# Kernel tuning notes

Measured on AMD Instinct MI355X. Metric: run time of the kernel, lower is better.

## Reference

```python
import jax, jax.numpy as jnp
import numpy as np

EPS = 1e-5

def _conv1x1(x, w):
    # w: [out_ch, in_ch], x: [n, c, h, w] -> [n, out_ch, h, w]
    return jnp.einsum('oc,nchw->nohw', w, x)

def _bn_relu(x, g, b, m, v):
    # inference-mode BatchNorm2d followed by ReLU
    s = g * jax.lax.rsqrt(v + EPS)
    return jax.nn.relu(x * s[None, :, None, None] + (b - m * s)[None, :, None, None])

def setup_inputs() -> dict:
    N, C, H, W, Kc, K = 8, 512, 128, 128, 512, 19
    keys = iter(jax.random.split(jax.random.key(0), 64))
    d = {}
    d['x'] = jax.random.normal(next(keys), (N, C, H, W), jnp.float32)
    d['proxy'] = jax.random.normal(next(keys), (N, C, K, 1), jnp.float32)
    for nm, shp in [('wp1', (Kc, C)), ('wp2', (Kc, Kc)), ('wo1', (Kc, C)),
                    ('wo2', (Kc, Kc)), ('wd', (Kc, C)), ('wu', (C, Kc))]:
        d[nm] = jax.random.normal(next(keys), shp, jnp.float32) * np.float32(1.0 / np.sqrt(shp[1]))
    for tag, ch in [('p1', Kc), ('p2', Kc), ('o1', Kc), ('o2', Kc), ('d', Kc), ('u', C)]:
        d['g' + tag] = 1.0 + 0.1 * jax.random.normal(next(keys), (ch,), jnp.float32)
        d['b' + tag] = 0.1 * jax.random.normal(next(keys), (ch,), jnp.float32)
        d['m' + tag] = 0.1 * jax.random.normal(next(keys), (ch,), jnp.float32)
        d['v' + tag] = jax.random.uniform(next(keys), (ch,), jnp.float32, 0.5, 1.5)
    return d

def reference(x, proxy,
              wp1, gp1, bp1, mp1, vp1, wp2, gp2, bp2, mp2, vp2,
              wo1, go1, bo1, mo1, vo1, wo2, go2, bo2, mo2, vo2,
              wd, gd, bd, md, vd, wu, gu, bu, mu, vu):
    # scale == 1: no pooling / upsampling
    # f_pixel: two 1x1 conv + BN + ReLU on pixel features
    q = _bn_relu(_conv1x1(x, wp1), gp1, bp1, mp1, vp1)
    q = _bn_relu(_conv1x1(q, wp2), gp2, bp2, mp2, vp2)        # [n, kc, h, w]
    n, kc, h, w = q.shape
    q = q.reshape(n, kc, h * w)                               # [n, kc, hw]
    # f_object on proxy (object region representations)
    k = _bn_relu(_conv1x1(proxy, wo1), go1, bo1, mo1, vo1)
    k = _bn_relu(_conv1x1(k, wo2), go2, bo2, mo2, vo2).reshape(n, kc, -1)  # [n, kc, K]
    # f_down (value)
    v = _bn_relu(_conv1x1(proxy, wd), gd, bd, md, vd).reshape(n, kc, -1)   # [n, kc, K]
    # cross-attention: pixels attend over object regions
    sim = jnp.einsum('ncq,nck->nqk', q, k) * (kc ** -0.5)     # [n, hw, K]
    attn = jax.nn.softmax(sim, axis=-1)
    ctx = jnp.einsum('nqk,nck->ncq', attn, v).reshape(n, kc, h, w)
    # f_up: 1x1 conv + BN + ReLU back to in_channels
    return _bn_relu(_conv1x1(ctx, wu), gu, bu, mu, vu)
```

## Files before the change

### kernel.cpp

```cpp
#include <hip/hip_runtime.h>
#include <stdint.h>

#define HW 16384
#define CH 512
#define KR 19

typedef float f32x4 __attribute__((ext_vector_type(4)));
typedef _Float16 half8 __attribute__((ext_vector_type(8)));
typedef unsigned short us8 __attribute__((ext_vector_type(8)));

__device__ __forceinline__ unsigned short f2h(float f) {
    union { _Float16 h; unsigned short u; } v; v.h = (_Float16)f; return v.u;
}
__device__ __forceinline__ float h2f(unsigned short u) {
    union { unsigned short u; _Float16 h; } v; v.u = u; return (float)v.h;
}

__global__ void ObjectAttentionBlock_1176821039805_kernel() {}

__global__ __launch_bounds__(256) void prep_kernel(
    const float* __restrict__ wp1, const float* __restrict__ wp2, const float* __restrict__ wu,
    unsigned short* __restrict__ wp1h, unsigned short* __restrict__ wp2h, unsigned short* __restrict__ wuh,
    const float* gp1, const float* bp1, const float* mp1, const float* vp1,
    const float* gp2, const float* bp2, const float* mp2, const float* vp2,
    const float* gu,  const float* bu,  const float* mu,  const float* vu,
    float* __restrict__ cons)
{
    int i = blockIdx.x * 256 + threadIdx.x;
    if (i < CH * CH) {
        wp1h[i] = f2h(wp1[i]);
        wp2h[i] = f2h(wp2[i]);
        wuh[i]  = f2h(wu[i]);
    }
    if (i < CH) {
        float s1 = gp1[i] * rsqrtf(vp1[i] + 1e-5f);
        cons[i] = s1;          cons[512 + i]  = bp1[i] - mp1[i] * s1;
        float s2 = gp2[i] * rsqrtf(vp2[i] + 1e-5f);
        cons[1024 + i] = s2;   cons[1536 + i] = bp2[i] - mp2[i] * s2;
        float su = gu[i] * rsqrtf(vu[i] + 1e-5f);
        cons[2048 + i] = su;   cons[2560 + i] = bu[i] - mu[i] * su;
    }
}

__global__ __launch_bounds__(256) void transpose_kernel(
    const float* __restrict__ x, unsigned short* __restrict__ xT)
{
    __shared__ unsigned short t[64][66];
    const int n  = blockIdx.z;
    const int c0 = blockIdx.y * 64;
    const int m0 = blockIdx.x * 64;
    const int tx = threadIdx.x & 63;
    const int ty = threadIdx.x >> 6;
    const float* xb = x + ((size_t)n * CH + c0) * HW + m0;
    #pragma unroll
    for (int r = 0; r < 16; ++r) {
        int cl = ty * 16 + r;
        t[cl][tx] = f2h(xb[(size_t)cl * HW + tx]);
    }
    __syncthreads();
    unsigned short* xo = xT + ((size_t)n * HW + m0) * CH + c0;
    #pragma unroll
    for (int r = 0; r < 16; ++r) {
        int ml = ty * 16 + r;
        xo[(size_t)ml * CH + tx] = t[tx][ml];
    }
}

__global__ __launch_bounds__(256) void kv1_kernel(
    const float* __restrict__ proxy, const float* __restrict__ wo1, const float* __restrict__ wd,
    const float* go1, const float* bo1, const float* mo1, const float* vo1,
    const float* gd,  const float* bd,  const float* md,  const float* vd,
    float* __restrict__ t1, float* __restrict__ vout)
{
    const int n  = blockIdx.x;
    const int o0 = blockIdx.y * 64;
    const float* px = proxy + (size_t)n * CH * KR;
    for (int idx = threadIdx.x; idx < 64 * KR; idx += 256) {
        int o = o0 + idx / KR;
        int j = idx % KR;
        float a1 = 0.f, a2 = 0.f;
        for (int c = 0; c < CH; ++c) {
            float p = px[c * KR + j];
            a1 += wo1[o * CH + c] * p;
            a2 += wd [o * CH + c] * p;
        }
        float s1 = go1[o] * rsqrtf(vo1[o] + 1e-5f);
        float s2 = gd[o]  * rsqrtf(vd[o]  + 1e-5f);
        t1  [((size_t)n * CH + o) * KR + j] = fmaxf(a1 * s1 + (bo1[o] - mo1[o] * s1), 0.f);
        vout[((size_t)n * CH + o) * KR + j] = fmaxf(a2 * s2 + (bd[o]  - md[o]  * s2), 0.f);
    }
}

__global__ __launch_bounds__(256) void kv2_kernel(
    const float* __restrict__ t1, const float* __restrict__ wo2,
    const float* go2, const float* bo2, const float* mo2, const float* vo2,
    float* __restrict__ kout)
{
    const int n  = blockIdx.x;
    const int o0 = blockIdx.y * 64;
    const float* tb = t1 + (size_t)n * CH * KR;
    for (int idx = threadIdx.x; idx < 64 * KR; idx += 256) {
        int o = o0 + idx / KR;
        int j = idx % KR;
        float a = 0.f;
        for (int c = 0; c < CH; ++c) a += wo2[o * CH + c] * tb[c * KR + j];
        float s = go2[o] * rsqrtf(vo2[o] + 1e-5f);
        kout[((size_t)n * CH + o) * KR + j] = fmaxf(a * s + (bo2[o] - mo2[o] * s), 0.f);
    }
}

__global__ __launch_bounds__(256) void pad_kernel(
    const float* __restrict__ kbuf, const float* __restrict__ vbuf,
    unsigned short* __restrict__ kt, unsigned short* __restrict__ vt)
{
    int idx = blockIdx.x * 256 + threadIdx.x;
    int n = idx >> 16, rem = idx & 65535;
    int j = rem >> 9, c = rem & 511;
    kt[idx] = (j < KR) ? f2h(kbuf[((size_t)(n * CH + c)) * KR + j]) : (unsigned short)0;
    int c2 = rem >> 7, j2 = rem & 127;
    vt[idx] = (j2 < KR) ? f2h(vbuf[((size_t)(n * CH + c2)) * KR + j2]) : (unsigned short)0;
}

template<int MODE, int KTILES, int NOUT, int BN>
__global__ __launch_bounds__(256) void gemm_nt(
    const unsigned short* __restrict__ A,
    const unsigned short* __restrict__ Wg, int wstride,
    const float* __restrict__ sc, const float* __restrict__ sh,
    void* __restrict__ outp)
{
    __shared__ __align__(16) char lds_raw[64 * 132 * 4];
    unsigned short* stage = (unsigned short*)lds_raw;
    float (*epi)[132] = (float (*)[132])lds_raw;

    const int KEL  = KTILES * 64;
    const int tid  = threadIdx.x;
    const int lane = tid & 63;
    const int wm = (tid >> 7) & 1;
    const int wn = (tid >> 6) & 1;
    const int i0 = blockIdx.x * 128;
    const int j0 = blockIdx.y * 128;
    const unsigned short* W = Wg + (size_t)(i0 >> 14) * wstride;

    size_t gA[4], gW[4];
    int ldso[4];
    #pragma unroll
    for (int q = 0; q < 4; ++q) {
        int ca = q * 256 + tid;
        int r = ca >> 3, p = ca & 7;
        gA[q] = (size_t)(i0 + r) * KEL + p * 8;
        gW[q] = (size_t)(j0 + r) * KEL + p * 8;
        ldso[q] = r * 64 + ((p ^ (r & 7)) << 3);
    }

    us8 va[4], vb[4];
    #pragma unroll
    for (int q = 0; q < 4; ++q) {
        va[q] = *(const us8*)(A + gA[q]);
        vb[q] = *(const us8*)(W + gW[q]);
    }

    const f32x4 zero = {0.f, 0.f, 0.f, 0.f};
    f32x4 acc[4][4];
    #pragma unroll
    for (int i = 0; i < 4; ++i)
        #pragma unroll
        for (int j = 0; j < 4; ++j) acc[i][j] = zero;

    const int arow = wm * 64 + (lane & 15);
    const int brow = wn * 64 + (lane & 15);
    const int kch  = lane >> 4;

    for (int kk = 0; kk < KTILES; ++kk) {
        __syncthreads();
        #pragma unroll
        for (int q = 0; q < 4; ++q) {
            *(us8*)(stage + ldso[q]) = va[q];
            *(us8*)(stage + 8192 + ldso[q]) = vb[q];
        }
        __syncthreads();
        if (kk < KTILES - 1) {
            #pragma unroll
            for (int q = 0; q < 4; ++q) {
                va[q] = *(const us8*)(A + gA[q] + (kk + 1) * 64);
                vb[q] = *(const us8*)(W + gW[q] + (kk + 1) * 64);
            }
        }
        #pragma unroll
        for (int s = 0; s < 2; ++s) {
            half8 af[4], bw[4];
            #pragma unroll
            for (int t = 0; t < 4; ++t) {
                int ra = arow + t * 16;
                af[t] = *(const half8*)(stage + ra * 64 + (((s * 4 + kch) ^ (ra & 7)) << 3));
                int rb = brow + t * 16;
                bw[t] = *(const half8*)(stage + 8192 + rb * 64 + (((s * 4 + kch) ^ (rb & 7)) << 3));
            }
            #pragma unroll
            for (int i = 0; i < 4; ++i)
                #pragma unroll
                for (int j = 0; j < 4; ++j)
                    acc[i][j] = __builtin_amdgcn_mfma_f32_16x16x32_f16(af[i], bw[j], acc[i][j], 0, 0, 0);
        }
    }

    float scv[4], shv[4];
    #pragma unroll
    for (int j = 0; j < 4; ++j) {
        int gj = j0 + wn * 64 + j * 16 + (lane & 15);
        scv[j] = BN ? sc[gj] : 1.0f;
        shv[j] = BN ? sh[gj] : 0.0f;
    }

    if (MODE == 0) {
        unsigned short* op = (unsigned short*)outp;
        #pragma unroll
        for (int i = 0; i < 4; ++i) {
            int gi = i0 + wm * 64 + i * 16 + (lane >> 4) * 4;
            #pragma unroll
            for (int j = 0; j < 4; ++j) {
                int gj = j0 + wn * 64 + j * 16 + (lane & 15);
                #pragma unroll
                for (int r = 0; r < 4; ++r) {
                    float vv = acc[i][j][r];
                    if (BN) vv = fmaxf(vv * scv[j] + shv[j], 0.f);
                    op[(size_t)(gi + r) * NOUT + gj] = f2h(vv);
                }
            }
        }
    } else if (MODE == 2) {
        float* op = (float*)outp;
        #pragma unroll
        for (int i = 0; i < 4; ++i) {
            int gi = i0 + wm * 64 + i * 16 + (lane >> 4) * 4;
            #pragma unroll
            for (int j = 0; j < 4; ++j) {
                int gj = j0 + wn * 64 + j * 16 + (lane & 15);
                #pragma unroll
                for (int r = 0; r < 4; ++r)
                    op[(size_t)(gi + r) * NOUT + gj] = acc[i][j][r];
            }
        }
    } else {
        float* op = (float*)outp;
        const int n  = i0 >> 14;
        const int mb = i0 & (HW - 1);
        #pragma unroll
        for (int h = 0; h < 2; ++h) {
            __syncthreads();
            if (wn == h) {
                #pragma unroll
                for (int j = 0; j < 4; ++j) {
                    int ljh = j * 16 + (lane & 15);
                    #pragma unroll
                    for (int i = 0; i < 4; ++i) {
                        int li = wm * 64 + i * 16 + (lane >> 4) * 4;
                        f32x4 vv;
                        #pragma unroll
                        for (int r = 0; r < 4; ++r)
                            vv[r] = fmaxf(acc[i][j][r] * scv[j] + shv[j], 0.f);
                        *(f32x4*)&epi[ljh][li] = vv;
                    }
                }
            }
            __syncthreads();
            #pragma unroll
            for (int q = 0; q < 8; ++q) {
                int idx = q * 256 + tid;
                int ch = idx >> 5, chunk = idx & 31;
                f32x4 v = *(const f32x4*)&epi[ch][chunk * 4];
                size_t base = ((size_t)(n * 512 + j0 + h * 64 + ch) << 14) + mb + chunk * 4;
                op[base] = v[0]; op[base + 1] = v[1]; op[base + 2] = v[2]; op[base + 3] = v[3];
            }
        }
    }
}

__global__ __launch_bounds__(256) void softmax_kernel(
    const float* __restrict__ sim, unsigned short* __restrict__ att)
{
    const size_t row = (size_t)blockIdx.x * 256 + threadIdx.x;
    const float* s = sim + row * 128;
    unsigned short* a = att + row * 128;
    const float scale = 0.044194173824159216f;
    float v[KR];
    float mx = -1e30f;
    #pragma unroll
    for (int j = 0; j < KR; ++j) { v[j] = s[j] * scale; mx = fmaxf(mx, v[j]); }
    float ssum = 0.f;
    #pragma unroll
    for (int j = 0; j < KR; ++j) { v[j] = __expf(v[j] - mx); ssum += v[j]; }
    const float inv = 1.0f / ssum;
    us8 o0, o1, o2;
    const us8 zz = {0, 0, 0, 0, 0, 0, 0, 0};
    #pragma unroll
    for (int e = 0; e < 8; ++e) { o0[e] = f2h(v[e] * inv); o1[e] = f2h(v[8 + e] * inv); }
    o2 = zz;
    o2[0] = f2h(v[16] * inv); o2[1] = f2h(v[17] * inv); o2[2] = f2h(v[18] * inv);
    *(us8*)(a) = o0;
    *(us8*)(a + 8) = o1;
    *(us8*)(a + 16) = o2;
    #pragma unroll
    for (int q = 3; q < 16; ++q) *(us8*)(a + q * 8) = zz;
}

extern "C" void kernel_launch(void* const* d_in, const int* in_sizes, int n_in,
                              void* d_out, int out_size, void* d_ws, size_t ws_size,
                              hipStream_t stream)
{
    const float* x     = (const float*)d_in[0];
    const float* proxy = (const float*)d_in[1];
    const float* wp1   = (const float*)d_in[2];
    const float* wp2   = (const float*)d_in[3];
    const float* wo1   = (const float*)d_in[4];
    const float* wo2   = (const float*)d_in[5];
    const float* wd    = (const float*)d_in[6];
    const float* wu    = (const float*)d_in[7];
    const float* gp1 = (const float*)d_in[8],  *bp1 = (const float*)d_in[9];
    const float* mp1 = (const float*)d_in[10], *vp1 = (const float*)d_in[11];
    const float* gp2 = (const float*)d_in[12], *bp2 = (const float*)d_in[13];
    const float* mp2 = (const float*)d_in[14], *vp2 = (const float*)d_in[15];
    const float* go1 = (const float*)d_in[16], *bo1 = (const float*)d_in[17];
    const float* mo1 = (const float*)d_in[18], *vo1 = (const float*)d_in[19];
    const float* go2 = (const float*)d_in[20], *bo2 = (const float*)d_in[21];
    const float* mo2 = (const float*)d_in[22], *vo2 = (const float*)d_in[23];
    const float* gd  = (const float*)d_in[24], *bd  = (const float*)d_in[25];
    const float* md  = (const float*)d_in[26], *vd  = (const float*)d_in[27];
    const float* gu  = (const float*)d_in[28], *bu  = (const float*)d_in[29];
    const float* mu  = (const float*)d_in[30], *vu  = (const float*)d_in[31];

    char* ws = (char*)d_ws;
    unsigned short* r0   = (unsigned short*)ws;
    unsigned short* wp1h = (unsigned short*)(ws + 134217728);
    unsigned short* wp2h = wp1h + 262144;
    unsigned short* wuh  = wp2h + 262144;
    float* t1   = (float*)(wuh + 262144);
    float* kbuf = t1 + 8 * CH * KR;
    float* vbuf = kbuf + 8 * CH * KR;
    float* cons = vbuf + 8 * CH * KR;

    float* outf = (float*)d_out;
    unsigned short* outh = (unsigned short*)d_out;
    unsigned short* q1T   = outh;
    float*          simb  = outf + 33554432;
    unsigned short* attb  = outh + 100663296;
    unsigned short* ktb   = outh + 117440512;
    unsigned short* vtb   = outh + 117964800;

    prep_kernel<<<1024, 256, 0, stream>>>(wp1, wp2, wu, wp1h, wp2h, wuh,
        gp1, bp1, mp1, vp1, gp2, bp2, mp2, vp2, gu, bu, mu, vu, cons);
    transpose_kernel<<<dim3(256, 8, 8), 256, 0, stream>>>(x, r0);
    kv1_kernel<<<dim3(8, 8), 256, 0, stream>>>(proxy, wo1, wd,
        go1, bo1, mo1, vo1, gd, bd, md, vd, t1, vbuf);
    kv2_kernel<<<dim3(8, 8), 256, 0, stream>>>(t1, wo2, go2, bo2, mo2, vo2, kbuf);

    gemm_nt<0, 8, 512, 1><<<dim3(1024, 4), 256, 0, stream>>>(r0, wp1h, 0, cons, cons + 512, q1T);
    gemm_nt<0, 8, 512, 1><<<dim3(1024, 4), 256, 0, stream>>>(q1T, wp2h, 0, cons + 1024, cons + 1536, r0);

    pad_kernel<<<2048, 256, 0, stream>>>(kbuf, vbuf, ktb, vtb);
    gemm_nt<2, 8, 128, 0><<<dim3(1024, 1), 256, 0, stream>>>(r0, ktb, 65536, cons, cons, simb);
    softmax_kernel<<<512, 256, 0, stream>>>(simb, attb);
    gemm_nt<0, 2, 512, 0><<<dim3(1024, 4), 256, 0, stream>>>(attb, vtb, 65536, cons, cons, r0);

    gemm_nt<1, 8, 512, 1><<<dim3(1024, 4), 256, 0, stream>>>(r0, wuh, 0, cons + 2048, cons + 2560, outf);
}
```

Measured before the change: 754.7 us.

## Fuse similarity, softmax and context GEMMs into one attention kernel; swizzle GEMM blocks

Replaces the three-step attention (q·k GEMM to an fp32 sim buffer, a separate softmax kernel, then an attn·v GEMM) with one kernel per 128-pixel tile. That kernel computes the 19-wide logits with MFMA, does the softmax with lane shuffles in registers, stages the probabilities and V in LDS, and writes the fp16 context in place. This removes the round trips through global memory for the large sim and attention buffers, plus two kernel launches. The generic GEMM is also specialised to K=512 and given a 1D grid with a block-index swizzle, meant to improve L2 reuse of A tiles across the four output-column blocks. The fused kernel writes its output unvectorised and runs with low MFMA occupancy.

Measured after the change: 735.4 us. -2.6%, faster.

```diff
diff --git a/kernel.cpp b/kernel.cpp
--- a/kernel.cpp
+++ b/kernel.cpp
@@ -8,6 +8,7 @@
 typedef float f32x4 __attribute__((ext_vector_type(4)));
 typedef _Float16 half8 __attribute__((ext_vector_type(8)));
 typedef unsigned short us8 __attribute__((ext_vector_type(8)));
+typedef unsigned short us4 __attribute__((ext_vector_type(4)));
 
 __device__ __forceinline__ unsigned short f2h(float f) {
     union { _Float16 h; unsigned short u; } v; v.h = (_Float16)f; return v.u;
@@ -121,10 +122,10 @@
     vt[idx] = (j2 < KR) ? f2h(vbuf[((size_t)(n * CH + c2)) * KR + j2]) : (unsigned short)0;
 }
 
-template<int MODE, int KTILES, int NOUT, int BN>
+template<int MODE, int BN>
 __global__ __launch_bounds__(256) void gemm_nt(
     const unsigned short* __restrict__ A,
-    const unsigned short* __restrict__ Wg, int wstride,
+    const unsigned short* __restrict__ W,
     const float* __restrict__ sc, const float* __restrict__ sh,
     void* __restrict__ outp)
 {
@@ -132,14 +133,14 @@
     unsigned short* stage = (unsigned short*)lds_raw;
     float (*epi)[132] = (float (*)[132])lds_raw;
 
-    const int KEL  = KTILES * 64;
     const int tid  = threadIdx.x;
     const int lane = tid & 63;
     const int wm = (tid >> 7) & 1;
     const int wn = (tid >> 6) & 1;
-    const int i0 = blockIdx.x * 128;
-    const int j0 = blockIdx.y * 128;
-    const unsigned short* W = Wg + (size_t)(i0 >> 14) * wstride;
+    const int id  = blockIdx.x;
+    const int swz = (id & 7) * 512 + (id >> 3);
+    const int i0 = (swz >> 2) << 7;
+    const int j0 = (swz & 3) << 7;
 
     size_t gA[4], gW[4];
     int ldso[4];
@@ -147,8 +148,8 @@
     for (int q = 0; q < 4; ++q) {
         int ca = q * 256 + tid;
         int r = ca >> 3, p = ca & 7;
-        gA[q] = (size_t)(i0 + r) * KEL + p * 8;
-        gW[q] = (size_t)(j0 + r) * KEL + p * 8;
+        gA[q] = (size_t)(i0 + r) * 512 + p * 8;
+        gW[q] = (size_t)(j0 + r) * 512 + p * 8;
         ldso[q] = r * 64 + ((p ^ (r & 7)) << 3);
     }
 
@@ -159,18 +160,17 @@
         vb[q] = *(const us8*)(W + gW[q]);
     }
 
-    const f32x4 zero = {0.f, 0.f, 0.f, 0.f};
     f32x4 acc[4][4];
     #pragma unroll
     for (int i = 0; i < 4; ++i)
         #pragma unroll
-        for (int j = 0; j < 4; ++j) acc[i][j] = zero;
+        for (int j = 0; j < 4; ++j) acc[i][j] = (f32x4){0.f, 0.f, 0.f, 0.f};
 
     const int arow = wm * 64 + (lane & 15);
     const int brow = wn * 64 + (lane & 15);
     const int kch  = lane >> 4;
 
-    for (int kk = 0; kk < KTILES; ++kk) {
+    for (int kk = 0; kk < 8; ++kk) {
         __syncthreads();
         #pragma unroll
         for (int q = 0; q < 4; ++q) {
@@ -178,7 +178,7 @@
             *(us8*)(stage + 8192 + ldso[q]) = vb[q];
         }
         __syncthreads();
-        if (kk < KTILES - 1) {
+        if (kk < 7) {
             #pragma unroll
             for (int q = 0; q < 4; ++q) {
                 va[q] = *(const us8*)(A + gA[q] + (kk + 1) * 64);
@@ -223,21 +223,8 @@
                 for (int r = 0; r < 4; ++r) {
                     float vv = acc[i][j][r];
                     if (BN) vv = fmaxf(vv * scv[j] + shv[j], 0.f);
-                    op[(size_t)(gi + r) * NOUT + gj] = f2h(vv);
+                    op[(size_t)(gi + r) * 512 + gj] = f2h(vv);
                 }
-            }
-        }
-    } else if (MODE == 2) {
-        float* op = (float*)outp;
-        #pragma unroll
-        for (int i = 0; i < 4; ++i) {
-            int gi = i0 + wm * 64 + i * 16 + (lane >> 4) * 4;
-            #pragma unroll
-            for (int j = 0; j < 4; ++j) {
-                int gj = j0 + wn * 64 + j * 16 + (lane & 15);
-                #pragma unroll
-                for (int r = 0; r < 4; ++r)
-                    op[(size_t)(gi + r) * NOUT + gj] = acc[i][j][r];
             }
         }
     } else {
@@ -275,32 +262,159 @@
     }
 }
 
-__global__ __launch_bounds__(256) void softmax_kernel(
-    const float* __restrict__ sim, unsigned short* __restrict__ att)
-{
-    const size_t row = (size_t)blockIdx.x * 256 + threadIdx.x;
-    const float* s = sim + row * 128;
-    unsigned short* a = att + row * 128;
+__global__ __launch_bounds__(256) void attn_fused(
+    const unsigned short* __restrict__ q2,
+    const unsigned short* __restrict__ ktg,
+    const unsigned short* __restrict__ vtg,
+    unsigned short* __restrict__ ctx)
+{
+    __shared__ __align__(16) char lds[47104];
+    unsigned short* stage = (unsigned short*)lds;
+    unsigned short* vt_l  = (unsigned short*)lds;
+    unsigned short* att_l = (unsigned short*)(lds + 36864);
+
+    const int tid  = threadIdx.x;
+    const int lane = tid & 63;
+    const int w    = tid >> 6;
+    const int i0   = blockIdx.x * 128;
+    const int n    = blockIdx.x >> 7;
+    const unsigned short* KT = ktg + n * 65536;
+    const unsigned short* VT = vtg + n * 65536;
+
+    size_t gA[4]; int loA[4];
+    #pragma unroll
+    for (int q = 0; q < 4; ++q) {
+        int ca = q * 256 + tid;
+        int r = ca >> 3, p = ca & 7;
+        gA[q] = (size_t)(i0 + r) * 512 + p * 8;
+        loA[q] = r * 64 + ((p ^ (r & 7)) << 3);
+    }
+    const int rB = tid >> 3, pB = tid & 7;
+    const size_t gB = (size_t)rB * 512 + pB * 8;
+    const int loB = 8192 + rB * 64 + ((pB ^ (rB & 7)) << 3);
+
+    us8 va[4], vbk;
+    #pragma unroll
+    for (int q = 0; q < 4; ++q) va[q] = *(const us8*)(q2 + gA[q]);
+    vbk = *(const us8*)(KT + gB);
+
+    f32x4 acc[2][2];
+    #pragma unroll
+    for (int i = 0; i < 2; ++i)
+        #pragma unroll
+        for (int j = 0; j < 2; ++j) acc[i][j] = (f32x4){0.f, 0.f, 0.f, 0.f};
+
+    const int kch = lane >> 4;
+    for (int kk = 0; kk < 8; ++kk) {
+        __syncthreads();
+        #pragma unroll
+        for (int q = 0; q < 4; ++q) *(us8*)(stage + loA[q]) = va[q];
+        *(us8*)(stage + loB) = vbk;
+        __syncthreads();
+        if (kk < 7) {
+            #pragma unroll
+            for (int q = 0; q < 4; ++q) va[q] = *(const us8*)(q2 + gA[q] + (kk + 1) * 64);
+            vbk = *(const us8*)(KT + gB + (kk + 1) * 64);
+        }
+        #pragma unroll
+        for (int s = 0; s < 2; ++s) {
+            half8 af[2], bf[2];
+            #pragma unroll
+            for (int i = 0; i < 2; ++i) {
+                int ra = w * 32 + i * 16 + (lane & 15);
+                af[i] = *(const half8*)(stage + ra * 64 + (((s * 4 + kch) ^ (ra & 7)) << 3));
+            }
+            #pragma unroll
+            for (int t = 0; t < 2; ++t) {
+                int rb = t * 16 + (lane & 15);
+                bf[t] = *(const half8*)(stage + 8192 + rb * 64 + (((s * 4 + kch) ^ (rb & 7)) << 3));
+            }
+            #pragma unroll
+            for (int i = 0; i < 2; ++i)
+                #pragma unroll
+                for (int j = 0; j < 2; ++j)
+                    acc[i][j] = __builtin_amdgcn_mfma_f32_16x16x32_f16(af[i], bf[j], acc[i][j], 0, 0, 0);
+        }
+    }
+
     const float scale = 0.044194173824159216f;
-    float v[KR];
-    float mx = -1e30f;
-    #pragma unroll
-    for (int j = 0; j < KR; ++j) { v[j] = s[j] * scale; mx = fmaxf(mx, v[j]); }
-    float ssum = 0.f;
-    #pragma unroll
-    for (int j = 0; j < KR; ++j) { v[j] = __expf(v[j] - mx); ssum += v[j]; }
-    const float inv = 1.0f / ssum;
-    us8 o0, o1, o2;
-    const us8 zz = {0, 0, 0, 0, 0, 0, 0, 0};
-    #pragma unroll
-    for (int e = 0; e < 8; ++e) { o0[e] = f2h(v[e] * inv); o1[e] = f2h(v[8 + e] * inv); }
-    o2 = zz;
-    o2[0] = f2h(v[16] * inv); o2[1] = f2h(v[17] * inv); o2[2] = f2h(v[18] * inv);
-    *(us8*)(a) = o0;
-    *(us8*)(a + 8) = o1;
-    *(us8*)(a + 16) = o2;
-    #pragma unroll
-    for (int q = 3; q < 16; ++q) *(us8*)(a + q * 8) = zz;
+    const bool v1 = (lane & 15) < 3;
+    unsigned short a16[2][4][2];
+    #pragma unroll
+    for (int i = 0; i < 2; ++i) {
+        #pragma unroll
+        for (int r = 0; r < 4; ++r) {
+            float s0 = acc[i][0][r] * scale;
+            float s1v = acc[i][1][r] * scale;
+            float m = v1 ? fmaxf(s0, s1v) : s0;
+            m = fmaxf(m, __shfl_xor(m, 1));
+            m = fmaxf(m, __shfl_xor(m, 2));
+            m = fmaxf(m, __shfl_xor(m, 4));
+            m = fmaxf(m, __shfl_xor(m, 8));
+            float a0 = __expf(s0 - m);
+            float a1 = v1 ? __expf(s1v - m) : 0.f;
+            float sm = a0 + a1;
+            sm += __shfl_xor(sm, 1);
+            sm += __shfl_xor(sm, 2);
+            sm += __shfl_xor(sm, 4);
+            sm += __shfl_xor(sm, 8);
+            float inv = 1.0f / sm;
+            a16[i][r][0] = f2h(a0 * inv);
+            a16[i][r][1] = f2h(a1 * inv);
+        }
+    }
+    #pragma unroll
+    for (int i = 0; i < 2; ++i)
+        #pragma unroll
+        for (int r = 0; r < 4; ++r) {
+            int R = w * 32 + i * 16 + (lane >> 4) * 4 + r;
+            att_l[R * 40 + (lane & 15)]      = a16[i][r][0];
+            att_l[R * 40 + 16 + (lane & 15)] = a16[i][r][1];
+        }
+    __syncthreads();
+
+    #pragma unroll
+    for (int q = 0; q < 8; ++q) {
+        int id = q * 256 + tid;
+        int c = id >> 2, part = id & 3;
+        us8 v = *(const us8*)(VT + (size_t)c * 128 + part * 8);
+        *(us4*)(vt_l + c * 36 + part * 8)     = (us4){v[0], v[1], v[2], v[3]};
+        *(us4*)(vt_l + c * 36 + part * 8 + 4) = (us4){v[4], v[5], v[6], v[7]};
+    }
+    __syncthreads();
+
+    half8 a2[2];
+    #pragma unroll
+    for (int i = 0; i < 2; ++i) {
+        int R = w * 32 + i * 16 + (lane & 15);
+        a2[i] = *(const half8*)(att_l + R * 40 + (lane >> 4) * 8);
+    }
+    #pragma unroll
+    for (int jc = 0; jc < 4; ++jc) {
+        half8 bf[8];
+        #pragma unroll
+        for (int t = 0; t < 8; ++t) {
+            int c = jc * 128 + t * 16 + (lane & 15);
+            const unsigned short* pb = vt_l + c * 36 + (lane >> 4) * 8;
+            us4 lo = *(const us4*)(pb);
+            us4 hi = *(const us4*)(pb + 4);
+            us8 u = {lo[0], lo[1], lo[2], lo[3], hi[0], hi[1], hi[2], hi[3]};
+            bf[t] = *(half8*)&u;
+        }
+        #pragma unroll
+        for (int i = 0; i < 2; ++i) {
+            #pragma unroll
+            for (int t = 0; t < 8; ++t) {
+                f32x4 o = __builtin_amdgcn_mfma_f32_16x16x32_f16(
+                    a2[i], bf[t], (f32x4){0.f, 0.f, 0.f, 0.f}, 0, 0, 0);
+                int col = jc * 128 + t * 16 + (lane & 15);
+                int row = i0 + w * 32 + i * 16 + (lane >> 4) * 4;
+                #pragma unroll
+                for (int r = 0; r < 4; ++r)
+                    ctx[(size_t)(row + r) * 512 + col] = f2h(o[r]);
+            }
+        }
+    }
 }
 
 extern "C" void kernel_launch(void* const* d_in, const int* in_sizes, int n_in,
@@ -340,11 +454,9 @@
 
     float* outf = (float*)d_out;
     unsigned short* outh = (unsigned short*)d_out;
-    unsigned short* q1T   = outh;
-    float*          simb  = outf + 33554432;
-    unsigned short* attb  = outh + 100663296;
-    unsigned short* ktb   = outh + 117440512;
-    unsigned short* vtb   = outh + 117964800;
+    unsigned short* q1T = outh;
+    unsigned short* ktb = outh + 117440512;
+    unsigned short* vtb = outh + 117964800;
 
     prep_kernel<<<1024, 256, 0, stream>>>(wp1, wp2, wu, wp1h, wp2h, wuh,
         gp1, bp1, mp1, vp1, gp2, bp2, mp2, vp2, gu, bu, mu, vu, cons);
@@ -352,14 +464,10 @@
     kv1_kernel<<<dim3(8, 8), 256, 0, stream>>>(proxy, wo1, wd,
         go1, bo1, mo1, vo1, gd, bd, md, vd, t1, vbuf);
     kv2_kernel<<<dim3(8, 8), 256, 0, stream>>>(t1, wo2, go2, bo2, mo2, vo2, kbuf);
-
-    gemm_nt<0, 8, 512, 1><<<dim3(1024, 4), 256, 0, stream>>>(r0, wp1h, 0, cons, cons + 512, q1T);
-    gemm_nt<0, 8, 512, 1><<<dim3(1024, 4), 256, 0, stream>>>(q1T, wp2h, 0, cons + 1024, cons + 1536, r0);
-
     pad_kernel<<<2048, 256, 0, stream>>>(kbuf, vbuf, ktb, vtb);
-    gemm_nt<2, 8, 128, 0><<<dim3(1024, 1), 256, 0, stream>>>(r0, ktb, 65536, cons, cons, simb);
-    softmax_kernel<<<512, 256, 0, stream>>>(simb, attb);
-    gemm_nt<0, 2, 512, 0><<<dim3(1024, 4), 256, 0, stream>>>(attb, vtb, 65536, cons, cons, r0);
-
-    gemm_nt<1, 8, 512, 1><<<dim3(1024, 4), 256, 0, stream>>>(r0, wuh, 0, cons + 2048, cons + 2560, outf);
-}
+
+    gemm_nt<0, 1><<<4096, 256, 0, stream>>>(r0, wp1h, cons, cons + 512, q1T);
+    gemm_nt<0, 1><<<4096, 256, 0, stream>>>(q1T, wp2h, cons + 1024, cons + 1536, r0);
+    attn_fused<<<1024, 256, 0, stream>>>(r0, ktb, vtb, r0);
+    gemm_nt<1, 1><<<4096, 256, 0, stream>>>(r0, wuh, cons + 2048, cons + 2560, outf);
+}
```
